# Optimization experiments

Measured on AMD Instinct MI355X. Metric: run time of the kernel, lower is better.

The kernel has to match this reference:

```python
import jax, jax.numpy as jnp
import numpy as np

KS = 3        # opt.kernel_size
B = 8         # batch
T = 512       # total_length (frames)
CQ = 126      # motion channels
CK = 80       # music channels
H = 128       # hid_c
SLOPE = 0.2   # lrelu slope in ConvBlock
INF = jnp.float32(1e30)


def _conv_block(x, w, b):
    # x: [B, Cin, T]; w: [Cout, Cin, KS]; reflect pad, stride 1, lrelu
    xp = jnp.pad(x, ((0, 0), (0, 0), (1, 1)), mode='reflect')
    y = jax.lax.conv_general_dilated(xp, w, (1,), 'VALID',
                                     dimension_numbers=('NCH', 'OIH', 'NCH'))
    return jax.nn.leaky_relu(y + b[None, :, None], SLOPE)


def _encode(x, params):
    for w, b in params:
        x = _conv_block(x, w, b)
    return x  # [B, H, T]


def _dtw_single(d, L):
    # d: [M, N] cost matrix, L: scalar int valid length. Returns 0/1 path matrix.
    M, N = d.shape
    jcol = jnp.arange(N)
    # row 0: cumulative along j, predecessor is 'left' (choice 1)
    row0 = jnp.cumsum(d[0])
    ch0 = jnp.where(jcol == 0, -1, 1).astype(jnp.int32)

    def row_step(prev_row, d_row):
        p_diag = jnp.concatenate([jnp.full((1,), INF), prev_row[:-1]])

        def inner(left, xs):
            pd, pu, dij, j = xs
            m = jnp.minimum(jnp.minimum(pd, left), pu)
            # tie-break order matches numpy code: diag, then left, then up
            choice = jnp.where(pd == m, 0, jnp.where(left == m, 1, 2)).astype(jnp.int32)
            cost = m + dij
            cost = jnp.where(j == 0, pu + dij, cost)      # first column: from up
            choice = jnp.where(j == 0, 2, choice)
            return cost, (cost, choice)

        _, (crow, chrow) = jax.lax.scan(inner, INF, (p_diag, prev_row, d_row, jcol))
        return crow, chrow

    _, chs = jax.lax.scan(row_step, row0, d[1:])
    choices = jnp.concatenate([ch0[None], chs], axis=0)  # [M, N]

    path01 = jnp.zeros((M, N), jnp.float32).at[L - 1, L - 1].set(1.0)

    def bt_step(carry, _):
        ix, iy, p = carry
        active = (ix > 0) | (iy > 0)
        c = choices[ix, iy]
        nix = jnp.where(c == 0, ix - 1, jnp.where(c == 1, ix, ix - 1))
        niy = jnp.where(c == 0, iy - 1, jnp.where(c == 1, iy - 1, iy))
        nix = jnp.where(active, nix, ix)
        niy = jnp.where(active, niy, iy)
        p = p.at[nix, niy].set(jnp.where(active, 1.0, p[nix, niy]))
        return (nix, niy, p), None

    (_, _, path01), _ = jax.lax.scan(bt_step, (L - 1, L - 1, path01), None,
                                     length=2 * M - 2)
    return path01


def setup_inputs() -> dict:
    key = jax.random.key(0)
    ks = jax.random.split(key, 16)

    def w(k, o, i):
        return jax.random.normal(k, (o, i, KS), jnp.float32) * np.float32(np.sqrt(2.0 / (i * KS)))

    inp = {
        'vec': jax.random.normal(ks[0], (B, CQ, T), jnp.float32),
        'music': jax.random.normal(ks[1], (B, CK, T), jnp.float32),
        'real_length': jax.random.randint(ks[2], (B,), T // 2, T + 1, jnp.int32),
        'qw1': w(ks[3], CQ, CQ), 'qb1': jnp.zeros((CQ,), jnp.float32),
        'qw2': w(ks[4], H, CQ),  'qb2': jnp.zeros((H,), jnp.float32),
        'qw3': w(ks[5], H, H),   'qb3': jnp.zeros((H,), jnp.float32),
        'kw1': w(ks[6], CK, CK), 'kb1': jnp.zeros((CK,), jnp.float32),
        'kw2': w(ks[7], H, CK),  'kb2': jnp.zeros((H,), jnp.float32),
        'kw3': w(ks[8], H, H),   'kb3': jnp.zeros((H,), jnp.float32),
    }
    return inp


def reference(vec, music, real_length, qw1, qb1, qw2, qb2, qw3, qb3,
              kw1, kb1, kw2, kb2, kw3, kb3):
    # conv encoders (ConvBlock x3 each)
    q = _encode(vec, [(qw1, qb1), (qw2, qb2), (qw3, qb3)])    # [B, H, T]
    k = _encode(music, [(kw1, kb1), (kw2, kb2), (kw3, kb3)])  # [B, H, T]
    qf = q.transpose(0, 2, 1)  # [B, N, H] motion latent
    kf = k.transpose(0, 2, 1)  # [B, M, H] music latent
    # Euclidean_dist(music_feat=kf, motion_feat=qf): dist[b, m, n] = ||kf[b,m]-qf[b,n]||
    diff = kf[:, :, None, :] - qf[:, None, :, :]              # [B, M, N, H]
    dist = jnp.sqrt(jnp.sum(diff * diff, axis=-1))            # [B, M, N]
    dist = (dist - dist.min()) / (dist.max() - dist.min())    # global min-max norm
    path01 = jax.vmap(_dtw_single)(dist, real_length)         # [B, M, N]
    return (path01, dist)
```

## Files before the change

### kernel.cpp

```cpp
#include <hip/hip_runtime.h>
#include <hip/hip_bf16.h>

#define T_LEN 512
#define BATCH 8
#define HID 128
#define NSTEP 640

__global__ __launch_bounds__(256) void repack_all_kernel(
    const float* __restrict__ s0, const float* __restrict__ s1,
    const float* __restrict__ s2, const float* __restrict__ s3,
    const float* __restrict__ s4, const float* __restrict__ s5,
    float* __restrict__ out)
{
    int i = blockIdx.x * 256 + threadIdx.x;
    const float* src; int li; float* dst;
    if      (i < 15876) { src = s0; li = i;         dst = out;          }
    else if (i < 32004) { src = s1; li = i - 15876; dst = out + 63504;  }
    else if (i < 48388) { src = s2; li = i - 32004; dst = out + 128016; }
    else if (i < 54788) { src = s3; li = i - 48388; dst = out + 193552; }
    else if (i < 65028) { src = s4; li = i - 54788; dst = out + 219152; }
    else if (i < 81412) { src = s5; li = i - 65028; dst = out + 260112; }
    else return;
    float a = src[li * 3], b = src[li * 3 + 1], c = src[li * 3 + 2];
    *reinterpret_cast<float4*>(dst + li * 4) = make_float4(a, b, c, 0.0f);
}

__global__ __launch_bounds__(512) void conv_block_kernel(
    const float* __restrict__ x, const float* __restrict__ wp,
    const float* __restrict__ bias, float* __restrict__ y,
    int Cin, int Cout)
{
    __shared__ float xs[128 * 66];
    const int b   = blockIdx.z;
    const int t0  = blockIdx.x * 64;
    const int tid = threadIdx.x;
    const int tl  = tid & 63;

    const float* xb = x + (size_t)b * Cin * T_LEN;
    for (int idx = tid; idx < Cin * 66; idx += 512) {
        int ci = idx / 66;
        int tt = idx - ci * 66;
        int g  = t0 + tt - 1;
        g = (g < 0) ? 1 : (g >= T_LEN ? T_LEN - 2 : g);
        xs[idx] = xb[ci * T_LEN + g];
    }
    __syncthreads();

    const int wave = __builtin_amdgcn_readfirstlane(tid >> 6);
    const int co0  = blockIdx.y * 16 + 2 * wave;
    if (co0 < Cout) {
        const float* __restrict__ wq0 = wp + (size_t)co0 * Cin * 4;
        const float* __restrict__ wq1 = wq0 + Cin * 4;
        float acc0 = 0.0f, acc1 = 0.0f;
#pragma unroll 4
        for (int ci = 0; ci < Cin; ++ci) {
            float xm = xs[ci * 66 + tl];
            float x0 = xs[ci * 66 + tl + 1];
            float xp = xs[ci * 66 + tl + 2];
            const float4 w0 = *reinterpret_cast<const float4*>(wq0 + ci * 4);
            const float4 w1 = *reinterpret_cast<const float4*>(wq1 + ci * 4);
            acc0 = fmaf(w0.x, xm, acc0);
            acc0 = fmaf(w0.y, x0, acc0);
            acc0 = fmaf(w0.z, xp, acc0);
            acc1 = fmaf(w1.x, xm, acc1);
            acc1 = fmaf(w1.y, x0, acc1);
            acc1 = fmaf(w1.z, xp, acc1);
        }
        float v0 = acc0 + bias[co0];
        float v1 = acc1 + bias[co0 + 1];
        v0 = (v0 >= 0.0f) ? v0 : 0.2f * v0;
        v1 = (v1 >= 0.0f) ? v1 : 0.2f * v1;
        y[((size_t)b * Cout + co0) * T_LEN + t0 + tl]     = v0;
        y[((size_t)b * Cout + co0 + 1) * T_LEN + t0 + tl] = v1;
    }
}

__global__ __launch_bounds__(256) void dist_kernel(
    const float* __restrict__ q, const float* __restrict__ k,
    float* __restrict__ dist, unsigned* __restrict__ mm)
{
    __shared__ __align__(16) float ks[HID * 32];
    __shared__ __align__(16) float qs[HID * 32];
    __shared__ float red[8];

    const int b  = blockIdx.z;
    const int m0 = blockIdx.y * 32;
    const int n0 = blockIdx.x * 32;
    const int tid = threadIdx.x;

    const float* qb = q + (size_t)b * HID * T_LEN;
    const float* kb = k + (size_t)b * HID * T_LEN;

    for (int idx = tid; idx < HID * 32; idx += 256) {
        int h = idx >> 5, c = idx & 31;
        ks[idx] = kb[h * T_LEN + m0 + c];
        qs[idx] = qb[h * T_LEN + n0 + c];
    }
    __syncthreads();

    const int nn = tid & 31;
    const int mq = (tid >> 5) * 4;

    float a0 = 0.f, a1 = 0.f, a2 = 0.f, a3 = 0.f;
    for (int h = 0; h < HID; ++h) {
        float qv = qs[h * 32 + nn];
        const float4 kv = *reinterpret_cast<const float4*>(&ks[h * 32 + mq]);
        float d0 = kv.x - qv, d1 = kv.y - qv, d2 = kv.z - qv, d3 = kv.w - qv;
        a0 = fmaf(d0, d0, a0);
        a1 = fmaf(d1, d1, a1);
        a2 = fmaf(d2, d2, a2);
        a3 = fmaf(d3, d3, a3);
    }
    float v0 = sqrtf(a0), v1 = sqrtf(a1), v2 = sqrtf(a2), v3 = sqrtf(a3);

    float* drow = dist + ((size_t)b * T_LEN + m0 + mq) * T_LEN + n0 + nn;
    drow[0 * T_LEN] = v0;
    drow[1 * T_LEN] = v1;
    drow[2 * T_LEN] = v2;
    drow[3 * T_LEN] = v3;

    float mnv = fminf(fminf(v0, v1), fminf(v2, v3));
    float mxv = fmaxf(fmaxf(v0, v1), fmaxf(v2, v3));
#pragma unroll
    for (int off = 32; off >= 1; off >>= 1) {
        mnv = fminf(mnv, __shfl_xor(mnv, off, 64));
        mxv = fmaxf(mxv, __shfl_xor(mxv, off, 64));
    }
    int wid = tid >> 6;
    if ((tid & 63) == 0) { red[wid * 2] = mnv; red[wid * 2 + 1] = mxv; }
    __syncthreads();
    if (tid == 0) {
        float mn = fminf(fminf(red[0], red[2]), fminf(red[4], red[6]));
        float mx = fmaxf(fmaxf(red[1], red[3]), fmaxf(red[5], red[7]));
        atomicMin(&mm[0], __float_as_uint(mn));
        atomicMax(&mm[1], __float_as_uint(mx));
    }
}

__global__ __launch_bounds__(512) void norm_shear_kernel(
    float* __restrict__ dist, float* __restrict__ dsk,
    const unsigned* __restrict__ mm)
{
    __shared__ float tile[64][65];
    const float mn  = __uint_as_float(mm[0]);
    const float rng = __uint_as_float(mm[1]) - mn;
    const int b  = blockIdx.z;
    const int m0 = blockIdx.y * 64;
    const int n0 = blockIdx.x * 64;
    const int tid  = threadIdx.x;
    const int lane = tid & 63;
    const int wv   = tid >> 6;

    float* D = dist + (size_t)b * T_LEN * T_LEN;
#pragma unroll
    for (int r = 0; r < 8; ++r) {
        int lm = wv + r * 8;
        float v = (D[(m0 + lm) * T_LEN + n0 + lane] - mn) / rng;
        D[(m0 + lm) * T_LEN + n0 + lane] = v;
        tile[lm][lane] = v;
    }
    __syncthreads();

    float* dskb = dsk + (size_t)b * NSTEP * T_LEN;
    const int tbase = n0 + (m0 >> 2);
    const int pidx  = (lane & 7) * 64 + (m0 >> 3) + (lane >> 3);
#pragma unroll
    for (int it = 0; it < 10; ++it) {
        int t_local = wv + it * 8;
        int ln = t_local - 2 * (lane >> 3);
        if (t_local <= 78 && ln >= 0 && ln < 64)
            dskb[(size_t)(tbase + t_local) * T_LEN + pidx] = tile[lane][ln];
    }
}

__device__ __forceinline__ void gload_lds16(const float* g, float* l) {
    __builtin_amdgcn_global_load_lds(
        (const __attribute__((address_space(1))) unsigned*)g,
        (__attribute__((address_space(3))) unsigned*)l, 16, 0, 0);
}

#define STAGE(GG, BUFI) do {                                                  \
    const float* gsrc = dskb + (size_t)(GG) * 8 * T_LEN;                      \
    _Pragma("unroll")                                                         \
    for (int rr = 0; rr < 8; ++rr) {                                          \
        gload_lds16(gsrc + rr * T_LEN +   0 + p * 4, &dstage[BUFI][rr][0]);   \
        gload_lds16(gsrc + rr * T_LEN + 256 + p * 4, &dstage[BUFI][rr][256]); \
    }                                                                         \
} while (0)

#define PREF(ARR, BUFI, ROWN) do {                                            \
    _Pragma("unroll")                                                         \
    for (int u = 0; u < 8; ++u) ARR[u] = dstage[BUFI][ROWN][u * 64 + p];      \
} while (0)

#define DTW_STEP_A(T, ARR) do {                                               \
    int j = (T) - 2 * p;                                                      \
    float nut = __shfl_up(L[7], 1, 64);     \
    if ((unsigned)j < 512u) {                                                 \
        int sh = (j & 15) * 2;                                                \
        float cur, oldL, prevrow;                                             \
        unsigned ch;                                                          \
        if (p == 0) {                                                         \
            cur = (j == 0) ? ARR[0] : (L[0] + ARR[0]); ch = 1u;               \
        } else if (j == 0) {                                                  \
            cur = ut + ARR[0]; ch = 2u;                                       \
        } else {                                                              \
            float pd = dt, lf = L[0], pu = ut;                                \
            float m = fminf(fminf(pd, lf), pu);                               \
            ch = (pd == m) ? 0u : ((lf == m) ? 1u : 2u);                      \
            cur = m + ARR[0];                                                 \
        }                                                                     \
        oldL = L[0]; L[0] = cur; prevrow = cur; pk[0] |= ch << sh;            \
        _Pragma("unroll")                                                     \
        for (int u = 1; u < 8; ++u) {                                         \
            if (j == 0) { cur = prevrow + ARR[u]; ch = 2u; }                  \
            else {                                                            \
                float pd = oldL, lf = L[u], pu = prevrow;                     \
                float m = fminf(fminf(pd, lf), pu);                           \
                ch = (pd == m) ? 0u : ((lf == m) ? 1u : 2u);                  \
                cur = m + ARR[u];                                             \
            }                                                                 \
            oldL = L[u]; L[u] = cur; prevrow = cur; pk[u] |= ch << sh;        \
        }                                                                     \
        if ((j & 15) == 15) {                                                 \
            int w4 = (j >> 4) * 4;                                            \
            *reinterpret_cast<uint4*>(&cho[p * 256 + w4]) =                   \
                make_uint4(pk[0], pk[1], pk[2], pk[3]);                       \
            *reinterpret_cast<uint4*>(&cho[p * 256 + 128 + w4]) =             \
                make_uint4(pk[4], pk[5], pk[6], pk[7]);                       \
            pk[0] = pk[1] = pk[2] = pk[3] = 0u;                               \
            pk[4] = pk[5] = pk[6] = pk[7] = 0u;                               \
        }                                                                     \
    }                                                                         \
    dt = ut; ut = nut;                                                        \
} while (0)

__global__ __launch_bounds__(64) void dtw_wave_kernel(
    const float* __restrict__ dsk, const int* __restrict__ rlen,
    float* __restrict__ path)
{
    __shared__ float dstage[2][8][512];
    __shared__ unsigned cho[512 * 32];

    const int b = blockIdx.x;
    const int p = threadIdx.x;
    const float* dskb = dsk + (size_t)b * NSTEP * T_LEN;

    float L[8];
    float ut = 1e30f, dt = 1e30f;
#pragma unroll
    for (int u = 0; u < 8; ++u) L[u] = 1e30f;
    unsigned pk[8] = {0u, 0u, 0u, 0u, 0u, 0u, 0u, 0u};

    STAGE(0, 0);
    STAGE(1, 1);
    asm volatile("s_waitcnt vmcnt(16)" ::: "memory");

    float da[8], db[8];
    PREF(da, 0, 0);

    for (int g = 0; g < 80; ++g) {
        const int cbuf = g & 1, nbuf = cbuf ^ 1;
        const int t0 = g * 8;
        PREF(db, cbuf, 1); DTW_STEP_A(t0 + 0, da);
        PREF(da, cbuf, 2); DTW_STEP_A(t0 + 1, db);
        PREF(db, cbuf, 3); DTW_STEP_A(t0 + 2, da);
        PREF(da, cbuf, 4); DTW_STEP_A(t0 + 3, db);
        PREF(db, cbuf, 5); DTW_STEP_A(t0 + 4, da);
        PREF(da, cbuf, 6); DTW_STEP_A(t0 + 5, db);
        PREF(db, cbuf, 7); DTW_STEP_A(t0 + 6, da);
        DTW_STEP_A(t0 + 7, db);
        if (g + 2 < 80) {
            STAGE(g + 2, cbuf);
            asm volatile("s_waitcnt vmcnt(16)" ::: "memory");
        } else {
            asm volatile("s_waitcnt vmcnt(0)" ::: "memory");
        }
        if (g + 1 < 80) PREF(da, nbuf, 0);
    }

    __syncthreads();

    if (p == 0) {
        int Lr = rlen[b];
        int ix = Lr - 1, iy = Lr - 1;
        float* po = path + (size_t)b * T_LEN * T_LEN;
        po[ix * T_LEN + iy] = 1.0f;
        while (ix > 0 || iy > 0) {
            uint4 tw = *reinterpret_cast<const uint4*>(
                &cho[((ix >> 2) * 32 + (iy >> 4)) * 4]);
            int tr = ix >> 2, tc = iy >> 4;
            while (true) {
                int sel = ix & 3;
                unsigned wvv = (sel & 2) ? ((sel & 1) ? tw.w : tw.z)
                                         : ((sel & 1) ? tw.y : tw.x);
                int c = (wvv >> ((iy & 15) * 2)) & 3;
                ix -= (c != 1);
                iy -= (c != 2);
                po[ix * T_LEN + iy] = 1.0f;
                if (!(ix > 0 || iy > 0)) break;
                if ((ix >> 2) != tr || (iy >> 4) != tc) break;
            }
        }
    }
}

extern "C" void kernel_launch(void* const* d_in, const int* in_sizes, int n_in,
                              void* d_out, int out_size, void* d_ws, size_t ws_size,
                              hipStream_t stream)
{
    (void)in_sizes; (void)n_in; (void)out_size; (void)ws_size;

    const float* vec   = (const float*)d_in[0];
    const float* music = (const float*)d_in[1];
    const int*   rlen  = (const int*)  d_in[2];
    const float* qw1 = (const float*)d_in[3];  const float* qb1 = (const float*)d_in[4];
    const float* qw2 = (const float*)d_in[5];  const float* qb2 = (const float*)d_in[6];
    const float* qw3 = (const float*)d_in[7];  const float* qb3 = (const float*)d_in[8];
    const float* kw1 = (const float*)d_in[9];  const float* kb1 = (const float*)d_in[10];
    const float* kw2 = (const float*)d_in[11]; const float* kb2 = (const float*)d_in[12];
    const float* kw3 = (const float*)d_in[13]; const float* kb3 = (const float*)d_in[14];

    float* out = (float*)d_out;
    const size_t mat_elems = (size_t)BATCH * T_LEN * T_LEN;
    float* path_out = out;
    float* dist_out = out + mat_elems;

    char* ws = (char*)d_ws;
    const size_t bufB = (size_t)BATCH * HID * T_LEN * sizeof(float);
    float* dsk = (float*)ws;
    float* qA = (float*)(ws + 0 * bufB);
    float* qB = (float*)(ws + 1 * bufB);
    float* kA = (float*)(ws + 2 * bufB);
    float* kB = (float*)(ws + 3 * bufB);
    float* wrep = (float*)(ws + 4 * bufB);
    float* qw1p = wrep;
    float* qw2p = wrep + 63504;
    float* qw3p = wrep + 128016;
    float* kw1p = wrep + 193552;
    float* kw2p = wrep + 219152;
    float* kw3p = wrep + 260112;
    unsigned* mm = (unsigned*)(ws + 10485760);

    hipMemsetAsync(path_out, 0, mat_elems * sizeof(float), stream);
    hipMemsetAsync(mm, 0xFF, 4, stream);
    hipMemsetAsync(mm + 1, 0x00, 4, stream);

    repack_all_kernel<<<dim3((81412 + 255) / 256), dim3(256), 0, stream>>>(
        qw1, qw2, qw3, kw1, kw2, kw3, wrep);

    dim3 cb(512);
    conv_block_kernel<<<dim3(8, 8, 8), cb, 0, stream>>>(vec, qw1p, qb1, qA, 126, 126);
    conv_block_kernel<<<dim3(8, 8, 8), cb, 0, stream>>>(qA,  qw2p, qb2, qB, 126, 128);
    conv_block_kernel<<<dim3(8, 8, 8), cb, 0, stream>>>(qB,  qw3p, qb3, qA, 128, 128);
    conv_block_kernel<<<dim3(8, 5, 8), cb, 0, stream>>>(music, kw1p, kb1, kA, 80, 80);
    conv_block_kernel<<<dim3(8, 8, 8), cb, 0, stream>>>(kA,   kw2p, kb2, kB, 80, 128);
    conv_block_kernel<<<dim3(8, 8, 8), cb, 0, stream>>>(kB,   kw3p, kb3, kA, 128, 128);

    dist_kernel<<<dim3(16, 16, 8), dim3(256), 0, stream>>>(qA, kA, dist_out, mm);

    norm_shear_kernel<<<dim3(8, 8, 8), dim3(512), 0, stream>>>(dist_out, dsk, mm);

    dtw_wave_kernel<<<dim3(BATCH), dim3(64), 0, stream>>>(dsk, rlen, path_out);
}
```

Measured before the change: 576.4 us.

## Merge q/k conv encoders into dual launches and deepen DTW prefetch

The six per-layer conv launches become three dual launches, each handling the motion and music encoder layer for the same depth through a blockIdx.y split. This cuts launch count and improves GPU fill. The two small memsets for the min/max scratch move into the repack kernel. The DTW wavefront loop now uses four rotating prefetch register buffers, so LDS reads are issued two steps ahead and the last two steps overlap the next group's prefetch. This adds register pressure and issues out-of-range prefetches on the final iteration.

```diff
diff --git a/kernel.cpp b/kernel.cpp
--- a/kernel.cpp
+++ b/kernel.cpp
@@ -10,9 +10,10 @@
     const float* __restrict__ s0, const float* __restrict__ s1,
     const float* __restrict__ s2, const float* __restrict__ s3,
     const float* __restrict__ s4, const float* __restrict__ s5,
-    float* __restrict__ out)
+    float* __restrict__ out, unsigned* __restrict__ mm)
 {
     int i = blockIdx.x * 256 + threadIdx.x;
+    if (i == 81412) { mm[0] = 0xFFFFFFFFu; mm[1] = 0u; return; }
     const float* src; int li; float* dst;
     if      (i < 15876) { src = s0; li = i;         dst = out;          }
     else if (i < 32004) { src = s1; li = i - 15876; dst = out + 63504;  }
@@ -25,16 +26,27 @@
     *reinterpret_cast<float4*>(dst + li * 4) = make_float4(a, b, c, 0.0f);
 }
 
-__global__ __launch_bounds__(512) void conv_block_kernel(
-    const float* __restrict__ x, const float* __restrict__ wp,
-    const float* __restrict__ bias, float* __restrict__ y,
-    int Cin, int Cout)
+__global__ __launch_bounds__(512) void conv_dual_kernel(
+    const float* __restrict__ xq, const float* __restrict__ wpq,
+    const float* __restrict__ bq, float* __restrict__ yq, int CinQ, int CoutQ,
+    const float* __restrict__ xk, const float* __restrict__ wpk,
+    const float* __restrict__ bk, float* __restrict__ yk, int CinK, int CoutK,
+    int ntq)
 {
     __shared__ float xs[128 * 66];
     const int b   = blockIdx.z;
     const int t0  = blockIdx.x * 64;
     const int tid = threadIdx.x;
     const int tl  = tid & 63;
+
+    const bool isQ = ((int)blockIdx.y) < ntq;
+    const int  yt  = isQ ? blockIdx.y : (blockIdx.y - ntq);
+    const float* x  = isQ ? xq  : xk;
+    const float* wp = isQ ? wpq : wpk;
+    const float* bias = isQ ? bq : bk;
+    float* y = isQ ? yq : yk;
+    const int Cin  = isQ ? CinQ  : CinK;
+    const int Cout = isQ ? CoutQ : CoutK;
 
     const float* xb = x + (size_t)b * Cin * T_LEN;
     for (int idx = tid; idx < Cin * 66; idx += 512) {
@@ -47,7 +59,7 @@
     __syncthreads();
 
     const int wave = __builtin_amdgcn_readfirstlane(tid >> 6);
-    const int co0  = blockIdx.y * 16 + 2 * wave;
+    const int co0  = yt * 16 + 2 * wave;
     if (co0 < Cout) {
         const float* __restrict__ wq0 = wp + (size_t)co0 * Cin * 4;
         const float* __restrict__ wq1 = wq0 + Cin * 4;
@@ -256,27 +268,27 @@
     STAGE(1, 1);
     asm volatile("s_waitcnt vmcnt(16)" ::: "memory");
 
-    float da[8], db[8];
+    float da[8], db[8], dc[8], dd[8];
     PREF(da, 0, 0);
+    PREF(db, 0, 1);
 
     for (int g = 0; g < 80; ++g) {
         const int cbuf = g & 1, nbuf = cbuf ^ 1;
         const int t0 = g * 8;
-        PREF(db, cbuf, 1); DTW_STEP_A(t0 + 0, da);
-        PREF(da, cbuf, 2); DTW_STEP_A(t0 + 1, db);
-        PREF(db, cbuf, 3); DTW_STEP_A(t0 + 2, da);
-        PREF(da, cbuf, 4); DTW_STEP_A(t0 + 3, db);
-        PREF(db, cbuf, 5); DTW_STEP_A(t0 + 4, da);
-        PREF(da, cbuf, 6); DTW_STEP_A(t0 + 5, db);
-        PREF(db, cbuf, 7); DTW_STEP_A(t0 + 6, da);
-        DTW_STEP_A(t0 + 7, db);
+        PREF(dc, cbuf, 2); DTW_STEP_A(t0 + 0, da);
+        PREF(dd, cbuf, 3); DTW_STEP_A(t0 + 1, db);
+        PREF(da, cbuf, 4); DTW_STEP_A(t0 + 2, dc);
+        PREF(db, cbuf, 5); DTW_STEP_A(t0 + 3, dd);
+        PREF(dc, cbuf, 6); DTW_STEP_A(t0 + 4, da);
+        PREF(dd, cbuf, 7); DTW_STEP_A(t0 + 5, db);
         if (g + 2 < 80) {
             STAGE(g + 2, cbuf);
             asm volatile("s_waitcnt vmcnt(16)" ::: "memory");
         } else {
             asm volatile("s_waitcnt vmcnt(0)" ::: "memory");
         }
-        if (g + 1 < 80) PREF(da, nbuf, 0);
+        PREF(da, nbuf, 0); DTW_STEP_A(t0 + 6, dc);
+        PREF(db, nbuf, 1); DTW_STEP_A(t0 + 7, dd);
     }
 
     __syncthreads();
@@ -343,19 +355,17 @@
     unsigned* mm = (unsigned*)(ws + 10485760);
 
     hipMemsetAsync(path_out, 0, mat_elems * sizeof(float), stream);
-    hipMemsetAsync(mm, 0xFF, 4, stream);
-    hipMemsetAsync(mm + 1, 0x00, 4, stream);
-
-    repack_all_kernel<<<dim3((81412 + 255) / 256), dim3(256), 0, stream>>>(
-        qw1, qw2, qw3, kw1, kw2, kw3, wrep);
+
+    repack_all_kernel<<<dim3((81413 + 255) / 256), dim3(256), 0, stream>>>(
+        qw1, qw2, qw3, kw1, kw2, kw3, wrep, mm);
 
     dim3 cb(512);
-    conv_block_kernel<<<dim3(8, 8, 8), cb, 0, stream>>>(vec, qw1p, qb1, qA, 126, 126);
-    conv_block_kernel<<<dim3(8, 8, 8), cb, 0, stream>>>(qA,  qw2p, qb2, qB, 126, 128);
-    conv_block_kernel<<<dim3(8, 8, 8), cb, 0, stream>>>(qB,  qw3p, qb3, qA, 128, 128);
-    conv_block_kernel<<<dim3(8, 5, 8), cb, 0, stream>>>(music, kw1p, kb1, kA, 80, 80);
-    conv_block_kernel<<<dim3(8, 8, 8), cb, 0, stream>>>(kA,   kw2p, kb2, kB, 80, 128);
-    conv_block_kernel<<<dim3(8, 8, 8), cb, 0, stream>>>(kB,   kw3p, kb3, kA, 128, 128);
+    conv_dual_kernel<<<dim3(8, 13, 8), cb, 0, stream>>>(
+        vec, qw1p, qb1, qA, 126, 126, music, kw1p, kb1, kA, 80, 80, 8);
+    conv_dual_kernel<<<dim3(8, 16, 8), cb, 0, stream>>>(
+        qA, qw2p, qb2, qB, 126, 128, kA, kw2p, kb2, kB, 80, 128, 8);
+    conv_dual_kernel<<<dim3(8, 16, 8), cb, 0, stream>>>(
+        qB, qw3p, qb3, qA, 128, 128, kB, kw3p, kb3, kA, 128, 128, 8);
 
     dist_kernel<<<dim3(16, 16, 8), dim3(256), 0, stream>>>(qA, kA, dist_out, mm);
 
```

New measurement: 560.0 us. 1.03x faster.
